# Performance work log

Hardware: AMD Instinct MI355X
Metric: run time of the kernel (lower is better)

The kernel has to match this reference:

```python
import jax, jax.numpy as jnp
import numpy as np

QTZ_BETA = 0.25


def setup_inputs() -> dict:
    key = jax.random.key(0)
    k1, k2 = jax.random.split(key)
    z = jax.random.normal(k1, (65536, 1, 256), dtype=jnp.float32)
    codebook = jax.random.normal(k2, (4096, 256), dtype=jnp.float32)
    return {"z": z, "codebook": codebook}


def reference(z, codebook):
    """Hard VQ quantization: nearest-codebook lookup with straight-through
    estimator plus codebook commitment loss. Returns (z_q, codebook_loss,
    min_embed_ids)."""
    D = codebook.shape[-1]
    z_f = z.reshape(-1, D)  # [N, D]
    # Pairwise squared L2 distances via expansion: ||z||^2 - 2 z c^T + ||c||^2
    # (argmin is invariant to the monotone transform vs. torch.cdist's sqrt)
    d2 = (
        jnp.sum(z_f * z_f, axis=1, keepdims=True)  # [N, 1]
        - 2.0 * (z_f @ codebook.T)                 # [N, K]
        + jnp.sum(codebook * codebook, axis=1)     # [K]
    )
    min_embed_ids = jnp.argmin(d2, axis=1)  # [N]
    # one_hot @ codebook is exactly a gather of codebook rows
    z_q = jnp.take(codebook, min_embed_ids, axis=0).reshape(z.shape)
    # Straight-through estimator
    z_q = z + jax.lax.stop_gradient(z_q - z)
    # Codebook loss (uses the STE z_q, matching the torch code)
    codebook_loss = (
        jnp.mean((jax.lax.stop_gradient(z_q) - z) ** 2)
        + jnp.mean((z_q - jax.lax.stop_gradient(z)) ** 2) * QTZ_BETA
    )
    return (z_q, codebook_loss, min_embed_ids)
```

## Files before the change

kernel.cpp:

```cpp
#include <hip/hip_runtime.h>
#include <stdint.h>

typedef _Float16 f16;
typedef _Float16 f16x4 __attribute__((ext_vector_type(4)));
typedef _Float16 f16x8 __attribute__((ext_vector_type(8)));
typedef float f32x4 __attribute__((ext_vector_type(4)));
typedef unsigned long long u64;

#define D_DIM 256
#define K_CB 4096
#define N_ROWS 65536
#define BM 128
#define BN 128
#define N_TILES 32
#define LOSS_OFF 16777216
#define IDS_OFF 16777217
#define MAX_FIX 4096

#define WS_CHI 0
#define WS_CN 2097152
#define WS_CNT 2113536
#define WS_ROWS 2113600
#define WS_SLOTS 2129984

#define GL_LDS(g, s_) __builtin_amdgcn_global_load_lds( \
    (const __attribute__((address_space(1))) void*)(g), \
    (__attribute__((address_space(3))) void*)(s_), 16, 0, 0)

static __device__ __forceinline__ uint32_t f2u(float x) { union { float f; uint32_t u; } c; c.f = x; return c.u; }
static __device__ __forceinline__ float u2f(uint32_t x) { union { float f; uint32_t u; } c; c.u = x; return c.f; }
static __device__ __forceinline__ uint32_t umin_(uint32_t a, uint32_t b) { return a < b ? a : b; }
static __device__ __forceinline__ uint32_t umax_(uint32_t a, uint32_t b) { return a > b ? a : b; }
static __device__ __forceinline__ u64 d2u(double x) { union { double d; u64 u; } c; c.d = x; return c.u; }

static __device__ __forceinline__ uint32_t med3u(uint32_t a, uint32_t b, uint32_t c) {
    uint32_t d;
    asm("v_med3_u32 %0, %1, %2, %3" : "=v"(d) : "v"(a), "v"(b), "v"(c));
    return d;
}
static __device__ __forceinline__ uint32_t min3u(uint32_t a, uint32_t b, uint32_t c) {
    uint32_t d;
    asm("v_min3_u32 %0, %1, %2, %3" : "=v"(d) : "v"(a), "v"(b), "v"(c));
    return d;
}

#define INS3(s_, kk_) do { \
    const uint32_t kkv_ = (kk_); \
    const uint32_t n1_ = umin_(k1[s_], kkv_); \
    const uint32_t n2_ = med3u(kkv_, k1[s_], k2[s_]); \
    const uint32_t n3_ = med3u(kkv_, k2[s_], k3[s_]); \
    k1[s_] = n1_; k2[s_] = n2_; k3[s_] = n3_; \
} while (0)

__global__ __launch_bounds__(256) void k_prep_cb(const float* __restrict__ cb,
                                                 f16* __restrict__ chi,
                                                 float* __restrict__ cn,
                                                 uint32_t* __restrict__ cnt,
                                                 u64* __restrict__ slots,
                                                 float* __restrict__ loss_slot) {
    const int tid = threadIdx.x;
    const int w = tid >> 6, l = tid & 63;
    const int row = blockIdx.x * 4 + w;
    const float4 v = ((const float4*)cb)[row * 64 + l];
    f16x4 h4;
    h4[0] = (f16)v.x; h4[1] = (f16)v.y; h4[2] = (f16)v.z; h4[3] = (f16)v.w;
    float ss = v.x * v.x + v.y * v.y + v.z * v.z + v.w * v.w;
#pragma unroll
    for (int m = 32; m >= 1; m >>= 1) ss += __shfl_xor(ss, m);
    ((f16x4*)chi)[row * 64 + l] = h4;
    if (l == 0) cn[row] = ss;
    if (tid < 4) slots[blockIdx.x * 4 + tid] = 0xFFFFFFFFFFFFFFFFull;
    if (blockIdx.x == 0 && tid == 0) { *cnt = 0; *loss_slot = 0.0f; }
}

#define TILE_BODY(ACC, PREV, TILE) do { \
    const int tile_ = (TILE); \
    _Pragma("unroll") for (int j = 0; j < 4; ++j) cnCur[j] = cnNext[j]; \
    _Pragma("unroll") for (int j = 0; j < 4; ++j) { \
        const float base_ = cnCur[j] + 64.0f; \
        _Pragma("unroll") for (int i = 0; i < 4; ++i) \
            ACC[i][j] = (f32x4){base_, base_, base_, base_}; \
    } \
    const int prevColb_ = (tile_ - 1) * BN + wn * 64 + l15; \
    _Pragma("unroll") for (int kc = 0; kc < 8; ++kc) { \
        __syncthreads(); \
        const int step_ = tile_ * 8 + kc; \
        if (step_ + 1 < N_TILES * 8) { \
            const int nt_ = (step_ + 1) >> 3, nk_ = (step_ + 1) & 7; \
            const f16* gh_ = chi + nt_ * (BN * D_DIM) + nk_ * 32 + offE; \
            char* bb_ = smem + 65536 + ((kc + 1) & 1) * 8192 + w * 1024; \
            GL_LDS(gh_, bb_); \
            GL_LDS(gh_ + 16384, bb_ + 4096); \
        } \
        if (kc == 0) { \
            const int tn_ = (tile_ + 1 < N_TILES) ? tile_ + 1 : tile_; \
            _Pragma("unroll") for (int j = 0; j < 4; ++j) \
                cnNext[j] = cn[tn_ * BN + wn * 64 + j * 16 + l15]; \
        } \
        const char* bbase_ = smem + 65536 + (kc & 1) * 8192; \
        f16x8 ah[4], bh[4]; \
        _Pragma("unroll") for (int i = 0; i < 4; ++i) { \
            const int t_ = ((kc << 2) + qh) ^ rs[i]; \
            ah[i] = *(const f16x8*)(smem + rowb[i] + (t_ << 4)); \
        } \
        _Pragma("unroll") for (int j = 0; j < 4; ++j) \
            bh[j] = *(const f16x8*)(bbase_ + bcon[j]); \
        {  \
            const int pi_ = kc >> 1; \
            _Pragma("unroll") for (int jj = 0; jj < 2; ++jj) { \
                const int pj_ = (kc & 1) * 2 + jj; \
                const uint32_t col_ = (uint32_t)(prevColb_ + pj_ * 16); \
                _Pragma("unroll") for (int rr = 0; rr < 4; ++rr) { \
                    const uint32_t kk_ = (f2u(PREV[pi_][pj_][rr]) & 0xFFFFF000u) | col_; \
                    INS3(pi_ * 4 + rr, kk_); \
                } \
            } \
        } \
        _Pragma("unroll") for (int i = 0; i < 4; ++i) \
            _Pragma("unroll") for (int j = 0; j < 4; ++j) \
                ACC[i][j] = __builtin_amdgcn_mfma_f32_16x16x32_f16(ah[i], bh[j], ACC[i][j], 0, 0, 0); \
    } \
} while (0)

__global__ __launch_bounds__(256, 2) void k_main(const float* __restrict__ z,
                                                 const float* __restrict__ cb,
                                                 const f16* __restrict__ chi,
                                                 const float* __restrict__ cn,
                                                 uint32_t* __restrict__ cnt,
                                                 uint32_t* __restrict__ rows,
                                                 float* __restrict__ out) {
    extern __shared__ char smem[];
    const int tid = threadIdx.x;
    const int w = tid >> 6, l = tid & 63;
    const int wm = w >> 1, wn = w & 1;
    const int l15 = l & 15, qh = l >> 4;
    const int blk = blockIdx.x;
    const float* ztile = z + (size_t)blk * (BM * D_DIM);

#pragma unroll 4
    for (int p = 0; p < 32; ++p) {
        const int r = p * 4 + w;
        const float4 v = ((const float4*)ztile)[r * 64 + l];
        f16x4 h4;
        h4[0] = (f16)(v.x * -2.0f); h4[1] = (f16)(v.y * -2.0f);
        h4[2] = (f16)(v.z * -2.0f); h4[3] = (f16)(v.w * -2.0f);
        const int addr = r * 512 + ((((l >> 1) ^ (r & 7))) << 4) + ((l & 1) << 3);
        *(f16x4*)(smem + addr) = h4;
    }

    float cnNext[4];
#pragma unroll
    for (int j = 0; j < 4; ++j) cnNext[j] = cn[wn * 64 + j * 16 + l15];

    const int e0 = tid >> 2;
    const int q0 = (tid & 3) ^ ((e0 >> 1) & 3);
    const int offE = e0 * 256 + q0 * 8;

    int rowb[4], rs[4], bcon[4];
#pragma unroll
    for (int i = 0; i < 4; ++i) {
        const int r = wm * 64 + i * 16 + l15;
        rowb[i] = r * 512;
        rs[i] = r & 7;
    }
#pragma unroll
    for (int j = 0; j < 4; ++j) {
        const int e = wn * 64 + j * 16 + l15;
        bcon[j] = e * 64 + ((qh ^ ((e >> 1) & 3)) << 4);
    }

    {
        const f16* gh = chi + offE;
        char* bb = smem + 65536 + w * 1024;
        GL_LDS(gh, bb);
        GL_LDS(gh + 16384, bb + 4096);
    }

    uint32_t k1[16], k2[16], k3[16];
#pragma unroll
    for (int s = 0; s < 16; ++s) { k1[s] = 0xFFFFFFFFu; k2[s] = 0xFFFFFFFFu; k3[s] = 0xFFFFFFFFu; }

    f32x4 accA[4][4], accB[4][4];
    {
        const float iv = __builtin_inff();
#pragma unroll
        for (int i = 0; i < 4; ++i)
#pragma unroll
            for (int j = 0; j < 4; ++j) accB[i][j] = (f32x4){iv, iv, iv, iv};
    }
    float cnCur[4];

    for (int tp = 0; tp < N_TILES; tp += 2) {
        TILE_BODY(accA, accB, tp);
        TILE_BODY(accB, accA, tp + 1);
    }
    {
        const int colb = (N_TILES - 1) * BN + wn * 64 + l15;
#pragma unroll
        for (int j = 0; j < 4; ++j) {
            const uint32_t col = (uint32_t)(colb + j * 16);
#pragma unroll
            for (int i = 0; i < 4; ++i)
#pragma unroll
                for (int rr = 0; rr < 4; ++rr) {
                    const uint32_t kk = (f2u(accB[i][j][rr]) & 0xFFFFF000u) | col;
                    INS3(i * 4 + rr, kk);
                }
        }
    }

#pragma unroll
    for (int s = 0; s < 16; ++s) {
        uint32_t a1 = k1[s], a2 = k2[s], a3 = k3[s];
#pragma unroll
        for (int m = 1; m <= 8; m <<= 1) {
            const uint32_t b1 = (uint32_t)__shfl_xor((int)a1, m);
            const uint32_t b2 = (uint32_t)__shfl_xor((int)a2, m);
            const uint32_t b3 = (uint32_t)__shfl_xor((int)a3, m);
            const uint32_t r1 = umin_(a1, b1);
            const uint32_t r2 = min3u(a2, b2, umax_(a1, b1));
            const uint32_t r3 = min3u(umax_(a1, b2), umax_(a2, b1), umin_(a3, b3));
            a1 = r1; a2 = r2; a3 = r3;
        }
        k1[s] = a1; k2[s] = a2; k3[s] = a3;
    }
    __syncthreads();
    uint32_t* mk = (uint32_t*)(smem + 65536);
    double* lossW = (double*)(smem + 65536 + 1536);
    if (wn == 0 && l15 == 0) {
#pragma unroll
        for (int s = 0; s < 16; ++s) {
            const int row = wm * 64 + (s >> 2) * 16 + qh * 4 + (s & 3);
            mk[row] = k1[s]; mk[128 + row] = k2[s]; mk[256 + row] = k3[s];
        }
    }
    __syncthreads();
    if (wn == 1 && l15 == 0) {
#pragma unroll
        for (int s = 0; s < 16; ++s) {
            const int row = wm * 64 + (s >> 2) * 16 + qh * 4 + (s & 3);
            const uint32_t b1 = mk[row], b2 = mk[128 + row], b3 = mk[256 + row];
            mk[row] = umin_(k1[s], b1);
            mk[128 + row] = min3u(k2[s], b2, umax_(k1[s], b1));
            mk[256 + row] = min3u(umax_(k1[s], b2), umax_(k2[s], b1), umin_(k3[s], b3));
        }
    }
    __syncthreads();

    double lossAcc = 0.0;
    for (int it = 0; it < 32; ++it) {
        const int row = it * 4 + w;
        const uint32_t K1 = mk[row], K2 = mk[128 + row], K3 = mk[256 + row];
        const int col1 = (int)(K1 & 4095u), col2 = (int)(K2 & 4095u);
        const float4 c1 = ((const float4*)cb)[col1 * 64 + l];
        const float4 c2 = ((const float4*)cb)[col2 * 64 + l];
        const float4 z4 = ((const float4*)ztile)[row * 64 + l];
        double e1, e2;
        {
            const double dx1 = (double)c1.x - z4.x, dy1 = (double)c1.y - z4.y;
            const double dz1 = (double)c1.z - z4.z, dw1 = (double)c1.w - z4.w;
            e1 = dx1 * dx1 + dy1 * dy1 + dz1 * dz1 + dw1 * dw1;
            const double dx2 = (double)c2.x - z4.x, dy2 = (double)c2.y - z4.y;
            const double dz2 = (double)c2.z - z4.z, dw2 = (double)c2.w - z4.w;
            e2 = dx2 * dx2 + dy2 * dy2 + dz2 * dz2 + dw2 * dw2;
        }
        float zn2 = z4.x * z4.x + z4.y * z4.y + z4.z * z4.z + z4.w * z4.w;
#pragma unroll
        for (int m = 32; m >= 1; m >>= 1) {
            e1 += __shfl_xor(e1, m);
            e2 += __shfl_xor(e2, m);
            zn2 += __shfl_xor(zn2, m);
        }
        const bool take1 = (e1 < e2) || (e1 == e2 && col1 <= col2);
        const float4 cw = take1 ? c1 : c2;
        ((float4*)out)[(blk * BM + row) * 64 + l] = cw;
        if (l == 0) {
            const int colw = take1 ? col1 : col2;
            const double ew = take1 ? e1 : e2;
            out[IDS_OFF + blk * BM + row] = (float)colw;
            lossAcc += ew;
            const float d3 = u2f(K3 & 0xFFFFF000u) + zn2 - 64.0f;
            const float eps = 0.006f * sqrtf(zn2) + 0.01f;
            if (!((float)ew < d3 - eps)) {
                const uint32_t e = atomicAdd(cnt, 1u);
                if (e < MAX_FIX) rows[e] = (uint32_t)(blk * BM + row);
            }
        }
    }
    if (l == 0) lossW[w] = lossAcc;
    __syncthreads();
    if (tid == 0) {
        const double tot = (lossW[0] + lossW[1] + lossW[2] + lossW[3]) * (1.25 / 16777216.0);
        atomicAdd(out + LOSS_OFF, (float)tot);
    }
}

__global__ __launch_bounds__(256) void k_fix_scan(const float* __restrict__ z,
                                                  const float* __restrict__ cb,
                                                  const uint32_t* __restrict__ cnt,
                                                  const uint32_t* __restrict__ rows,
                                                  u64* __restrict__ slots) {
    __shared__ float zrow[256];
    __shared__ u64 wmin[4];
    const int tid = threadIdx.x;
    const int w = tid >> 6, l = tid & 63;
    const int chunk = blockIdx.x & 15;
    uint32_t n = *cnt; if (n > MAX_FIX) n = MAX_FIX;
    for (uint32_t e = blockIdx.x >> 4; e < n; e += 64) {
        const int row = (int)rows[e];
        __syncthreads();
        if (tid < 64) ((float4*)zrow)[tid] = ((const float4*)z)[row * 64 + tid];
        __syncthreads();
        const int c = chunk * 256 + tid;
        const float4* crow = (const float4*)(cb + (size_t)c * 256);
        double s = 0.0;
        for (int q = 0; q < 64; ++q) {
            const float4 cv = crow[q];
            const float4 zv = ((const float4*)zrow)[q];
            const double dx = (double)cv.x - zv.x, dy = (double)cv.y - zv.y;
            const double dz = (double)cv.z - zv.z, dw = (double)cv.w - zv.w;
            s += dx * dx + dy * dy + dz * dz + dw * dw;
        }
        u64 key = (d2u(s) & 0xFFFFFFFFFFFFF000ull) | (u64)c;
#pragma unroll
        for (int m = 32; m >= 1; m >>= 1) {
            const u64 o = __shfl_xor(key, m);
            if (o < key) key = o;
        }
        if (l == 0) wmin[w] = key;
        __syncthreads();
        if (tid == 0) {
            u64 k = wmin[0];
            if (wmin[1] < k) k = wmin[1];
            if (wmin[2] < k) k = wmin[2];
            if (wmin[3] < k) k = wmin[3];
            atomicMin(&slots[e], k);
        }
    }
}

__global__ __launch_bounds__(256) void k_fix_patch(const float* __restrict__ z,
                                                   const float* __restrict__ cb,
                                                   const uint32_t* __restrict__ cnt,
                                                   const uint32_t* __restrict__ rows,
                                                   const u64* __restrict__ slots,
                                                   float* __restrict__ out) {
    const int tid = threadIdx.x;
    uint32_t n = *cnt; if (n > MAX_FIX) n = MAX_FIX;
    for (uint32_t e = blockIdx.x; e < n; e += 256) {
        const int row = (int)rows[e];
        const int newc = (int)(slots[e] & 4095ull);
        const int oldc = (int)out[IDS_OFF + row];
        if (newc == oldc) continue;
        double dOld = 0.0, dNew = 0.0;
        if (tid < 64) {
            const float4 zv = ((const float4*)z)[row * 64 + tid];
            const float4 co = ((const float4*)cb)[oldc * 64 + tid];
            const float4 cn4 = ((const float4*)cb)[newc * 64 + tid];
            const double ax = (double)co.x - zv.x, ay = (double)co.y - zv.y;
            const double az = (double)co.z - zv.z, aw = (double)co.w - zv.w;
            dOld = ax * ax + ay * ay + az * az + aw * aw;
            const double bx = (double)cn4.x - zv.x, by = (double)cn4.y - zv.y;
            const double bz = (double)cn4.z - zv.z, bw = (double)cn4.w - zv.w;
            dNew = bx * bx + by * by + bz * bz + bw * bw;
            ((float4*)out)[row * 64 + tid] = cn4;
        }
#pragma unroll
        for (int m = 32; m >= 1; m >>= 1) {
            dOld += __shfl_xor(dOld, m);
            dNew += __shfl_xor(dNew, m);
        }
        if (tid == 0) {
            out[IDS_OFF + row] = (float)newc;
            atomicAdd(out + LOSS_OFF, (float)((dNew - dOld) * (1.25 / 16777216.0)));
        }
    }
}

extern "C" void kernel_launch(void* const* d_in, const int* in_sizes, int n_in,
                              void* d_out, int out_size, void* d_ws, size_t ws_size,
                              hipStream_t stream) {
    (void)in_sizes; (void)n_in; (void)out_size; (void)ws_size;
    const float* z = (const float*)d_in[0];
    const float* cb = (const float*)d_in[1];
    float* out = (float*)d_out;
    char* ws = (char*)d_ws;
    f16* chi = (f16*)(ws + WS_CHI);
    float* cn = (float*)(ws + WS_CN);
    uint32_t* cnt = (uint32_t*)(ws + WS_CNT);
    uint32_t* rows = (uint32_t*)(ws + WS_ROWS);
    u64* slots = (u64*)(ws + WS_SLOTS);

    hipFuncSetAttribute((const void*)k_main,
                        hipFuncAttributeMaxDynamicSharedMemorySize, 81920);

    k_prep_cb<<<K_CB / 4, 256, 0, stream>>>(cb, chi, cn, cnt, slots, out + LOSS_OFF);
    k_main<<<N_ROWS / BM, 256, 81920, stream>>>(z, cb, chi, cn, cnt, rows, out);
    k_fix_scan<<<1024, 256, 0, stream>>>(z, cb, cnt, rows, slots);
    k_fix_patch<<<256, 256, 0, stream>>>(z, cb, cnt, rows, slots, out);
}
```

Before: 295.8 us.

## Load codebook fragments directly to registers, drop LDS staging and per-step barriers

```diff
diff --git a/kernel.cpp b/kernel.cpp
--- a/kernel.cpp
+++ b/kernel.cpp
@@ -23,9 +23,7 @@
 #define WS_ROWS 2113600
 #define WS_SLOTS 2129984
 
-#define GL_LDS(g, s_) __builtin_amdgcn_global_load_lds( \
-    (const __attribute__((address_space(1))) void*)(g), \
-    (__attribute__((address_space(3))) void*)(s_), 16, 0, 0)
+#define LDS_BYTES 67584
 
 static __device__ __forceinline__ uint32_t f2u(float x) { union { float f; uint32_t u; } c; c.f = x; return c.u; }
 static __device__ __forceinline__ float u2f(uint32_t x) { union { float f; uint32_t u; } c; c.u = x; return c.f; }
@@ -83,28 +81,26 @@
     } \
     const int prevColb_ = (tile_ - 1) * BN + wn * 64 + l15; \
     _Pragma("unroll") for (int kc = 0; kc < 8; ++kc) { \
-        __syncthreads(); \
-        const int step_ = tile_ * 8 + kc; \
-        if (step_ + 1 < N_TILES * 8) { \
-            const int nt_ = (step_ + 1) >> 3, nk_ = (step_ + 1) & 7; \
-            const f16* gh_ = chi + nt_ * (BN * D_DIM) + nk_ * 32 + offE; \
-            char* bb_ = smem + 65536 + ((kc + 1) & 1) * 8192 + w * 1024; \
-            GL_LDS(gh_, bb_); \
-            GL_LDS(gh_ + 16384, bb_ + 4096); \
+        const int cur_ = kc & 1, nxt_ = cur_ ^ 1; \
+        if (tile_ * 8 + kc + 1 < N_TILES * 8) { \
+            if (kc < 7) { \
+                _Pragma("unroll") for (int j = 0; j < 4; ++j) \
+                    bh[nxt_][j] = *(const f16x8*)(bpc[j] + (kc + 1) * 64); \
+            } else { \
+                _Pragma("unroll") for (int j = 0; j < 4; ++j) { \
+                    bpc[j] += 65536; \
+                    bh[nxt_][j] = *(const f16x8*)bpc[j]; \
+                } \
+            } \
         } \
         if (kc == 0) { \
             const int tn_ = (tile_ + 1 < N_TILES) ? tile_ + 1 : tile_; \
             _Pragma("unroll") for (int j = 0; j < 4; ++j) \
                 cnNext[j] = cn[tn_ * BN + wn * 64 + j * 16 + l15]; \
         } \
-        const char* bbase_ = smem + 65536 + (kc & 1) * 8192; \
-        f16x8 ah[4], bh[4]; \
-        _Pragma("unroll") for (int i = 0; i < 4; ++i) { \
-            const int t_ = ((kc << 2) + qh) ^ rs[i]; \
-            ah[i] = *(const f16x8*)(smem + rowb[i] + (t_ << 4)); \
-        } \
-        _Pragma("unroll") for (int j = 0; j < 4; ++j) \
-            bh[j] = *(const f16x8*)(bbase_ + bcon[j]); \
+        f16x8 ah[4]; \
+        _Pragma("unroll") for (int i = 0; i < 4; ++i) \
+            ah[i] = *(const f16x8*)(smem + ab + kc * 8192 + i * 1024); \
         {  \
             const int pi_ = kc >> 1; \
             _Pragma("unroll") for (int jj = 0; jj < 2; ++jj) { \
@@ -116,9 +112,11 @@
                 } \
             } \
         } \
+        __builtin_amdgcn_s_setprio(1); \
         _Pragma("unroll") for (int i = 0; i < 4; ++i) \
             _Pragma("unroll") for (int j = 0; j < 4; ++j) \
-                ACC[i][j] = __builtin_amdgcn_mfma_f32_16x16x32_f16(ah[i], bh[j], ACC[i][j], 0, 0, 0); \
+                ACC[i][j] = __builtin_amdgcn_mfma_f32_16x16x32_f16(ah[i], bh[cur_][j], ACC[i][j], 0, 0, 0); \
+        __builtin_amdgcn_s_setprio(0); \
     } \
 } while (0)
 
@@ -137,6 +135,15 @@
     const int blk = blockIdx.x;
     const float* ztile = z + (size_t)blk * (BM * D_DIM);
 
+    const char* bpc[4];
+#pragma unroll
+    for (int j = 0; j < 4; ++j)
+        bpc[j] = (const char*)(chi + (size_t)(wn * 64 + j * 16 + l15) * 256 + qh * 8);
+
+    f16x8 bh[2][4];
+#pragma unroll
+    for (int j = 0; j < 4; ++j) bh[0][j] = *(const f16x8*)bpc[j];
+
 #pragma unroll 4
     for (int p = 0; p < 32; ++p) {
         const int r = p * 4 + w;
@@ -144,7 +151,8 @@
         f16x4 h4;
         h4[0] = (f16)(v.x * -2.0f); h4[1] = (f16)(v.y * -2.0f);
         h4[2] = (f16)(v.z * -2.0f); h4[3] = (f16)(v.w * -2.0f);
-        const int addr = r * 512 + ((((l >> 1) ^ (r & 7))) << 4) + ((l & 1) << 3);
+        const int kcw = l >> 3, q = (l >> 1) & 3, half = l & 1;
+        const int addr = kcw * 8192 + r * 64 + (((q ^ ((r >> 1) & 3))) << 4) + half * 8;
         *(f16x4*)(smem + addr) = h4;
     }
 
@@ -152,29 +160,7 @@
 #pragma unroll
     for (int j = 0; j < 4; ++j) cnNext[j] = cn[wn * 64 + j * 16 + l15];
 
-    const int e0 = tid >> 2;
-    const int q0 = (tid & 3) ^ ((e0 >> 1) & 3);
-    const int offE = e0 * 256 + q0 * 8;
-
-    int rowb[4], rs[4], bcon[4];
-#pragma unroll
-    for (int i = 0; i < 4; ++i) {
-        const int r = wm * 64 + i * 16 + l15;
-        rowb[i] = r * 512;
-        rs[i] = r & 7;
-    }
-#pragma unroll
-    for (int j = 0; j < 4; ++j) {
-        const int e = wn * 64 + j * 16 + l15;
-        bcon[j] = e * 64 + ((qh ^ ((e >> 1) & 3)) << 4);
-    }
-
-    {
-        const f16* gh = chi + offE;
-        char* bb = smem + 65536 + w * 1024;
-        GL_LDS(gh, bb);
-        GL_LDS(gh + 16384, bb + 4096);
-    }
+    const int ab = wm * 4096 + l15 * 64 + ((qh ^ ((l15 >> 1) & 3)) << 4);
 
     uint32_t k1[16], k2[16], k3[16];
 #pragma unroll
@@ -189,6 +175,8 @@
             for (int j = 0; j < 4; ++j) accB[i][j] = (f32x4){iv, iv, iv, iv};
     }
     float cnCur[4];
+
+    __syncthreads();
 
     for (int tp = 0; tp < N_TILES; tp += 2) {
         TILE_BODY(accA, accB, tp);
@@ -224,9 +212,9 @@
         }
         k1[s] = a1; k2[s] = a2; k3[s] = a3;
     }
-    __syncthreads();
     uint32_t* mk = (uint32_t*)(smem + 65536);
     double* lossW = (double*)(smem + 65536 + 1536);
+    __syncthreads();
     if (wn == 0 && l15 == 0) {
 #pragma unroll
         for (int s = 0; s < 16; ++s) {
@@ -392,10 +380,10 @@
     u64* slots = (u64*)(ws + WS_SLOTS);
 
     hipFuncSetAttribute((const void*)k_main,
-                        hipFuncAttributeMaxDynamicSharedMemorySize, 81920);
+                        hipFuncAttributeMaxDynamicSharedMemorySize, LDS_BYTES);
 
     k_prep_cb<<<K_CB / 4, 256, 0, stream>>>(cb, chi, cn, cnt, slots, out + LOSS_OFF);
-    k_main<<<N_ROWS / BM, 256, 81920, stream>>>(z, cb, chi, cn, cnt, rows, out);
+    k_main<<<N_ROWS / BM, 256, LDS_BYTES, stream>>>(z, cb, chi, cn, cnt, rows, out);
     k_fix_scan<<<1024, 256, 0, stream>>>(z, cb, cnt, rows, slots);
     k_fix_patch<<<256, 256, 0, stream>>>(z, cb, cnt, rows, slots, out);
 }
```

Result: slower. 393.1 us (+32.9%).
